# Optimization experiments

Measured on AMD Instinct MI355X. Metric: run time of the kernel, lower is better.

The kernel has to match this reference:

```python
import jax, jax.numpy as jnp
import numpy as np

HIDDEN = 1024
HEADS = 16
HEAD_DIM = HIDDEN // HEADS
SCALE = HEAD_DIM ** -0.5


def setup_inputs() -> dict:
    key = jax.random.key(0)
    ks = jax.random.split(key, 7)
    B, N, T = 4, 64, 128
    x = jax.random.normal(ks[0], (B * N, T, HIDDEN), dtype=jnp.float32)
    bvecs = jax.random.normal(ks[1], (B, T, 3), dtype=jnp.float32)
    w_std = HIDDEN ** -0.5
    qkv_w = jax.random.normal(ks[2], (HIDDEN, 3 * HIDDEN), dtype=jnp.float32) * w_std
    qkv_b = jnp.zeros((3 * HIDDEN,), dtype=jnp.float32)
    proj_w = jax.random.normal(ks[3], (HIDDEN, HIDDEN), dtype=jnp.float32) * w_std
    proj_b = jnp.zeros((HIDDEN,), dtype=jnp.float32)
    angular_bias_scale = jnp.ones((1,), dtype=jnp.float32)
    return {"x": x, "bvecs": bvecs, "qkv_w": qkv_w, "qkv_b": qkv_b,
            "proj_w": proj_w, "proj_b": proj_b,
            "angular_bias_scale": angular_bias_scale}


def reference(x, bvecs, qkv_w, qkv_b, proj_w, proj_b, angular_bias_scale):
    BN, T, D = x.shape
    B = bvecs.shape[0]
    N = BN // B
    # QKV projection -> (3, BN, H, T, hd)
    qkv = (x @ qkv_w + qkv_b).reshape(BN, T, 3, HEADS, HEAD_DIM)
    qkv = jnp.transpose(qkv, (2, 0, 3, 1, 4))
    q, k, v = qkv[0], qkv[1], qkv[2]
    # normalize b-vectors and compute per-batch angular cosine similarity (B, T, T)
    bvecs_n = bvecs / (jnp.linalg.norm(bvecs, axis=-1, keepdims=True) + 1e-6)
    cos_sim = jnp.clip(jnp.einsum('bid,bjd->bij', bvecs_n, bvecs_n), -1.0, 1.0)
    # repeat across the N patches per batch -> (BN, 1, T, T)
    angular_bias = jnp.repeat(cos_sim, N, axis=0)[:, None, :, :]
    attn_logits = jnp.einsum('bhid,bhjd->bhij', q, k) * SCALE
    attn = jax.nn.softmax(attn_logits + angular_bias_scale * angular_bias, axis=-1)
    out = jnp.einsum('bhij,bhjd->bhid', attn, v)
    out = jnp.transpose(out, (0, 2, 1, 3)).reshape(BN, T, D)
    return out @ proj_w + proj_b
```

## Files before the change

### kernel.cpp

```cpp
#include <hip/hip_runtime.h>
#include <hip/hip_bf16.h>
#include <stdint.h>


typedef float f32x4 __attribute__((ext_vector_type(4)));
typedef __bf16 bf16x8 __attribute__((ext_vector_type(8)));
typedef unsigned short us8 __attribute__((ext_vector_type(8)));
typedef unsigned short u16;

#define MROWS 32768

static __device__ __forceinline__ u16 bfbits(float f) {
  __bf16 h = (__bf16)f;
  return __builtin_bit_cast(u16, h);
}
static __device__ __forceinline__ float bff(u16 u) {
  return (float)__builtin_bit_cast(__bf16, u);
}
static __device__ __forceinline__ void gld16(const void* g, void* l) {
  __builtin_amdgcn_global_load_lds(
      (const __attribute__((address_space(1))) void*)g,
      (__attribute__((address_space(3))) void*)l, 16, 0, 0);
}
static __device__ __forceinline__ f32x4 mfma16(bf16x8 a, bf16x8 b, f32x4 c) {
  return __builtin_amdgcn_mfma_f32_16x16x32_bf16(a, b, c, 0, 0, 0);
}

__global__ __launch_bounds__(256) void k_split(const float* __restrict__ x,
                                               u16* __restrict__ xhl, int n4) {
  int i = blockIdx.x * 256 + threadIdx.x;
  if (i >= n4) return;
  float4 v = ((const float4*)x)[i];
  ushort4 h, l;
  h.x = bfbits(v.x); l.x = bfbits(v.x - bff(h.x));
  h.y = bfbits(v.y); l.y = bfbits(v.y - bff(h.y));
  h.z = bfbits(v.z); l.z = bfbits(v.z - bff(h.z));
  h.w = bfbits(v.w); l.w = bfbits(v.w - bff(h.w));
  int i4 = i << 2;
  int r = i4 >> 10, k = i4 & 1023;
  size_t o = ((size_t)r << 11) + (size_t)((k >> 5) << 6) + (k & 31);
  *(ushort4*)(xhl + o) = h;
  *(ushort4*)(xhl + o + 32) = l;
}

__global__ void k_tsplit(const float* __restrict__ w, u16* __restrict__ thl,
                         int K, int N, int remap) {
  __shared__ float tile[32][33];
  int n0 = blockIdx.x * 32, k0 = blockIdx.y * 32;
  int tx = threadIdx.x, ty = threadIdx.y;
#pragma unroll
  for (int j = 0; j < 32; j += 8)
    tile[ty + j][tx] = w[(size_t)(k0 + ty + j) * N + n0 + tx];
  __syncthreads();
#pragma unroll
  for (int j = 0; j < 32; j += 8) {
    float v = tile[tx][ty + j];
    int n = n0 + ty + j;
    int orow = n;
    if (remap) {
      int s = n >> 10, hid = n & 1023;
      orow = (hid >> 8) * 768 + s * 256 + (hid & 255);
    }
    int k = k0 + tx;
    size_t o = ((size_t)orow << 11) + (size_t)((k >> 5) << 6) + (k & 31);
    u16 hb = bfbits(v);
    thl[o] = hb;
    thl[o + 32] = bfbits(v - bff(hb));
  }
}

__global__ void k_gbias(const float* __restrict__ b, float* __restrict__ gb) {
  int n = blockIdx.x * 256 + threadIdx.x;
  if (n >= 3072) return;
  int s = n >> 10, hid = n & 1023;
  gb[(hid >> 8) * 768 + s * 256 + (hid & 255)] = b[n];
}

__global__ void k_cos(const float* __restrict__ bv, float* __restrict__ cosb) {
  int b = blockIdx.x, t = threadIdx.x;
  __shared__ float nb[128][3];
  float x = bv[(b * 128 + t) * 3 + 0];
  float y = bv[(b * 128 + t) * 3 + 1];
  float z = bv[(b * 128 + t) * 3 + 2];
  float inv = 1.0f / (sqrtf(x * x + y * y + z * z) + 1e-6f);
  nb[t][0] = x * inv; nb[t][1] = y * inv; nb[t][2] = z * inv;
  __syncthreads();
  float xn = nb[t][0], yn = nb[t][1], zn = nb[t][2];
  for (int j = 0; j < 128; j++) {
    float c = xn * nb[j][0] + yn * nb[j][1] + zn * nb[j][2];
    c = fminf(1.0f, fmaxf(-1.0f, c));
    cosb[((size_t)b * 128 + t) * 128 + j] = c;
  }
}

template <int AMODE, int MODE>
__global__ __launch_bounds__(512, 2) void k_gemm(
    const u16* __restrict__ Ahl, const float* __restrict__ Af,
    const u16* __restrict__ Bhl, const float* __restrict__ bias,
    float* __restrict__ C) {
  __shared__ __align__(16) u16 sA[3][128 * 64];
  __shared__ __align__(16) u16 sB[3][256 * 64];
  int tid = threadIdx.x;
  int wave = tid >> 6, lane = tid & 63;
  int fr = lane & 15, fq = lane >> 4;
  int wm = wave >> 2, wn = wave & 3;

  int nT = gridDim.y;
  int h = blockIdx.y * gridDim.x + blockIdx.x;
  int nwg = gridDim.x * gridDim.y;
  int w = (h & 7) * (nwg >> 3) + (h >> 3);
  int rowBase = (w / nT) * 128, colBase = (w % nT) * 256;

  f32x4 acc[4][4];
#pragma unroll
  for (int i = 0; i < 4; i++)
#pragma unroll
    for (int j = 0; j < 4; j++) acc[i][j] = (f32x4){0.f, 0.f, 0.f, 0.f};

  int lr = lane >> 3, ls = (lane & 7) ^ lr;
  const u16* aS = Ahl + (size_t)(rowBase + lr) * 2048 + ls * 8;
  const u16* bS = Bhl + (size_t)(colBase + lr) * 2048 + ls * 8;

  auto stageB = [&](int t, int buf) {
#pragma unroll
    for (int q = 0; q < 4; q++) {
      int R = (q * 8 + wave) * 8;
      gld16(bS + (size_t)R * 2048 + t * 64, &sB[buf][R * 64]);
    }
  };
  auto stageA0 = [&](int t, int buf) {
#pragma unroll
    for (int q = 0; q < 2; q++) {
      int R = (q * 8 + wave) * 8;
      gld16(aS + (size_t)R * 2048 + t * 64, &sA[buf][R * 64]);
    }
  };
  auto stageA1 = [&](int t, int buf) {
    int row = tid >> 2, cs = tid & 3;
    const float* src = Af + (size_t)(rowBase + row) * 1024 + t * 32 + cs * 8;
    float4 v0 = *(const float4*)src;
    float4 v1 = *(const float4*)(src + 4);
    float vv[8] = {v0.x, v0.y, v0.z, v0.w, v1.x, v1.y, v1.z, v1.w};
    us8 hv, lv;
#pragma unroll
    for (int i = 0; i < 8; i++) {
      u16 hb = bfbits(vv[i]);
      hv[i] = hb;
      lv[i] = bfbits(vv[i] - bff(hb));
    }
    int sw = row & 7;
    *(us8*)(&sA[buf][row * 64 + ((cs ^ sw) << 3)]) = hv;
    *(us8*)(&sA[buf][row * 64 + (((cs + 4) ^ sw) << 3)]) = lv;
  };
  auto stage = [&](int t, int buf) {
    stageB(t, buf);
    if constexpr (AMODE == 0) stageA0(t, buf);
    else stageA1(t, buf);
  };

  auto tile = [&](int t, int cur, int nbuf, int vmode) {
    const u16* lA = &sA[cur][0];
    const u16* lB = &sB[cur][0];
    bf16x8 fbh[4], fbl[4];
#pragma unroll
    for (int ni = 0; ni < 4; ni++) {
      int c = wn * 64 + ni * 16 + fr;
      int sw = c & 7;
      fbh[ni] = *(const bf16x8*)(&lB[c * 64 + ((fq ^ sw) << 3)]);
      fbl[ni] = *(const bf16x8*)(&lB[c * 64 + (((fq + 4) ^ sw) << 3)]);
    }
    if (t + 2 < 32) stage(t + 2, nbuf);
#pragma unroll
    for (int mi = 0; mi < 4; mi++) {
      bf16x8 fah, fal;
      int r = wm * 64 + mi * 16 + fr;
      int sw = r & 7;
      fah = *(const bf16x8*)(&lA[r * 64 + ((fq ^ sw) << 3)]);
      fal = *(const bf16x8*)(&lA[r * 64 + (((fq + 4) ^ sw) << 3)]);
#pragma unroll
      for (int ni = 0; ni < 4; ni++) {
        acc[mi][ni] = mfma16(fah, fbh[ni], acc[mi][ni]);
        acc[mi][ni] = mfma16(fah, fbl[ni], acc[mi][ni]);
        acc[mi][ni] = mfma16(fal, fbh[ni], acc[mi][ni]);
      }
    }
    if constexpr (AMODE == 1) {
      if (vmode >= 0)
        asm volatile("s_waitcnt vmcnt(0) lgkmcnt(0)" ::: "memory");
    } else {
      if (vmode == 6)
        asm volatile("s_waitcnt vmcnt(6)" ::: "memory");
      else if (vmode == 0)
        asm volatile("s_waitcnt vmcnt(0)" ::: "memory");
    }
    __builtin_amdgcn_s_barrier();
  };

  stage(0, 0);
  stage(1, 1);
  if constexpr (AMODE == 0) {
    asm volatile("s_waitcnt vmcnt(6)" ::: "memory");
  } else {
    asm volatile("s_waitcnt vmcnt(0) lgkmcnt(0)" ::: "memory");
  }
  __builtin_amdgcn_s_barrier();

#pragma unroll 1
  for (int tb = 0; tb < 30; tb += 3) {
    tile(tb, 0, 2, 6);
    tile(tb + 1, 1, 0, 6);
    tile(tb + 2, 2, 1, 6);
  }
  tile(30, 0, 2, 0);
  tile(31, 1, 0, -1);

#pragma unroll
  for (int mi = 0; mi < 4; mi++)
#pragma unroll
    for (int ni = 0; ni < 4; ni++)
#pragma unroll
      for (int rr = 0; rr < 4; rr++) {
        int row = rowBase + wm * 64 + mi * 16 + fq * 4 + rr;
        int col = colBase + wn * 64 + ni * 16 + fr;
        float v = acc[mi][ni][rr] + bias[col];
        if constexpr (MODE == 0) {
          int s = col >> 8, hl2 = (col >> 6) & 3, d = col & 63;
          int bn = row >> 7, t = row & 127;
          size_t idx;
          if (s == 2)
            idx = ((size_t)(bn * 4 + hl2) * 64 + d) * 128 + t;
          else
            idx = ((size_t)(bn * 4 + hl2) * 128 + t) * 64 + d;
          C[(size_t)s * 8388608 + idx] = v;
        } else {
          C[(size_t)row * 1024 + col] = v;
        }
      }
}

__global__ __launch_bounds__(256) void k_attn(
    const float* __restrict__ Q, const float* __restrict__ Kb,
    const float* __restrict__ Vt, const float* __restrict__ cosb,
    const float* __restrict__ absSp, u16* __restrict__ Ohl, int g) {
  __shared__ __align__(16) u16 sQ[2][64 * 72];
  __shared__ __align__(16) u16 sKV[2][64 * 72];
  __shared__ __align__(16) float sS[64 * 132];
  u16* sP = (u16*)sS;

  int bx = blockIdx.x;
  int half = bx & 1, hl = (bx >> 1) & 3, bn = bx >> 3, b = bn >> 6;
  int tid = threadIdx.x, wave = tid >> 6, lane = tid & 63;
  int fr = lane & 15, fq = lane >> 4;
  size_t base = (size_t)(bn * 4 + hl) * 8192;
  float absS = absSp[0];

  {
    const float* src = Q + base + (size_t)half * 4096;
#pragma unroll
    for (int p = 0; p < 4; p++) {
      int f = p * 256 + tid, r = f >> 4, c = f & 15;
      float4 v = *(const float4*)(src + r * 64 + c * 4);
      ushort4 h, l;
      h.x = bfbits(v.x); l.x = bfbits(v.x - bff(h.x));
      h.y = bfbits(v.y); l.y = bfbits(v.y - bff(h.y));
      h.z = bfbits(v.z); l.z = bfbits(v.z - bff(h.z));
      h.w = bfbits(v.w); l.w = bfbits(v.w - bff(h.w));
      *(ushort4*)(&sQ[0][r * 72 + c * 4]) = h;
      *(ushort4*)(&sQ[1][r * 72 + c * 4]) = l;
    }
  }

  bf16x8 qh[2], ql[2];

#pragma unroll
  for (int kt = 0; kt < 2; kt++) {
    if (kt) __syncthreads();
    {
      const float* src = Kb + base + (size_t)kt * 4096;
#pragma unroll
      for (int p = 0; p < 4; p++) {
        int f = p * 256 + tid, r = f >> 4, c = f & 15;
        float4 v = *(const float4*)(src + r * 64 + c * 4);
        ushort4 h, l;
        h.x = bfbits(v.x); l.x = bfbits(v.x - bff(h.x));
        h.y = bfbits(v.y); l.y = bfbits(v.y - bff(h.y));
        h.z = bfbits(v.z); l.z = bfbits(v.z - bff(h.z));
        h.w = bfbits(v.w); l.w = bfbits(v.w - bff(h.w));
        *(ushort4*)(&sKV[0][r * 72 + c * 4]) = h;
        *(ushort4*)(&sKV[1][r * 72 + c * 4]) = l;
      }
    }
    __syncthreads();
    if (kt == 0) {
      int rowl = wave * 16 + fr;
#pragma unroll
      for (int ki = 0; ki < 2; ki++) {
        qh[ki] = *(const bf16x8*)(&sQ[0][rowl * 72 + ki * 32 + fq * 8]);
        ql[ki] = *(const bf16x8*)(&sQ[1][rowl * 72 + ki * 32 + fq * 8]);
      }
    }
#pragma unroll
    for (int nt = 0; nt < 4; nt++) {
      f32x4 a = (f32x4){0.f, 0.f, 0.f, 0.f};
      int cl = nt * 16 + fr;
#pragma unroll
      for (int ki = 0; ki < 2; ki++) {
        bf16x8 kh = *(const bf16x8*)(&sKV[0][cl * 72 + ki * 32 + fq * 8]);
        bf16x8 kl = *(const bf16x8*)(&sKV[1][cl * 72 + ki * 32 + fq * 8]);
        a = mfma16(qh[ki], kh, a);
        a = mfma16(qh[ki], kl, a);
        a = mfma16(ql[ki], kh, a);
      }
#pragma unroll
      for (int rr = 0; rr < 4; rr++) {
        int rl = wave * 16 + fq * 4 + rr;
        int col = kt * 64 + nt * 16 + fr;
        int tg = half * 64 + rl;
        float cv = cosb[((size_t)(b * 128 + tg)) * 128 + col];
        sS[rl * 132 + col] = a[rr] * 0.125f + absS * cv;
      }
    }
  }
  __syncthreads();

  {
    const float* src = Vt + base;
#pragma unroll
    for (int p = 0; p < 4; p++) {
      int f = p * 256 + tid, r = f >> 4, c = f & 15;
      float4 v = *(const float4*)(src + r * 128 + c * 4);
      ushort4 h, l;
      h.x = bfbits(v.x); l.x = bfbits(v.x - bff(h.x));
      h.y = bfbits(v.y); l.y = bfbits(v.y - bff(h.y));
      h.z = bfbits(v.z); l.z = bfbits(v.z - bff(h.z));
      h.w = bfbits(v.w); l.w = bfbits(v.w - bff(h.w));
      *(ushort4*)(&sKV[0][r * 72 + c * 4]) = h;
      *(ushort4*)(&sKV[1][r * 72 + c * 4]) = l;
    }
  }

  for (int r = 0; r < 16; r++) {
    int tl = wave * 16 + r;
    float s0 = sS[tl * 132 + lane], s1 = sS[tl * 132 + 64 + lane];
    float m = fmaxf(s0, s1);
#pragma unroll
    for (int off = 32; off >= 1; off >>= 1) m = fmaxf(m, __shfl_xor(m, off));
    float p0 = __expf(s0 - m), p1 = __expf(s1 - m);
    float sum = p0 + p1;
#pragma unroll
    for (int off = 32; off >= 1; off >>= 1) sum += __shfl_xor(sum, off);
    float inv = 1.0f / sum;
    p0 *= inv; p1 *= inv;
    u16 h0 = bfbits(p0), h1 = bfbits(p1);
    sP[tl * 264 + lane] = h0;
    sP[tl * 264 + 64 + lane] = h1;
    sP[tl * 264 + 128 + lane] = bfbits(p0 - bff(h0));
    sP[tl * 264 + 192 + lane] = bfbits(p1 - bff(h1));
  }

  f32x4 accO[4];
#pragma unroll
  for (int nt = 0; nt < 4; nt++) accO[nt] = (f32x4){0.f, 0.f, 0.f, 0.f};
#pragma unroll
  for (int vt = 0; vt < 2; vt++) {
    if (vt) {
      __syncthreads();
      const float* src = Vt + base + 64;
#pragma unroll
      for (int p = 0; p < 4; p++) {
        int f = p * 256 + tid, r = f >> 4, c = f & 15;
        float4 v = *(const float4*)(src + r * 128 + c * 4);
        ushort4 h, l;
        h.x = bfbits(v.x); l.x = bfbits(v.x - bff(h.x));
        h.y = bfbits(v.y); l.y = bfbits(v.y - bff(h.y));
        h.z = bfbits(v.z); l.z = bfbits(v.z - bff(h.z));
        h.w = bfbits(v.w); l.w = bfbits(v.w - bff(h.w));
        *(ushort4*)(&sKV[0][r * 72 + c * 4]) = h;
        *(ushort4*)(&sKV[1][r * 72 + c * 4]) = l;
      }
    }
    __syncthreads();
    int rowl = wave * 16 + fr;
    bf16x8 ph[2], pl[2];
#pragma unroll
    for (int ki = 0; ki < 2; ki++) {
      ph[ki] = *(const bf16x8*)(&sP[rowl * 264 + vt * 64 + ki * 32 + fq * 8]);
      pl[ki] = *(const bf16x8*)(&sP[rowl * 264 + 128 + vt * 64 + ki * 32 + fq * 8]);
    }
#pragma unroll
    for (int nt = 0; nt < 4; nt++) {
      int d = nt * 16 + fr;
#pragma unroll
      for (int ki = 0; ki < 2; ki++) {
        bf16x8 vh = *(const bf16x8*)(&sKV[0][d * 72 + ki * 32 + fq * 8]);
        bf16x8 vl = *(const bf16x8*)(&sKV[1][d * 72 + ki * 32 + fq * 8]);
        accO[nt] = mfma16(ph[ki], vh, accO[nt]);
        accO[nt] = mfma16(ph[ki], vl, accO[nt]);
        accO[nt] = mfma16(pl[ki], vh, accO[nt]);
      }
    }
  }

  int hg = g * 4 + hl;
#pragma unroll
  for (int nt = 0; nt < 4; nt++)
#pragma unroll
    for (int rr = 0; rr < 4; rr++) {
      int tl = wave * 16 + fq * 4 + rr;
      int tg = half * 64 + tl;
      int d = nt * 16 + fr;
      float v = accO[nt][rr];
      size_t o = ((size_t)(bn * 128 + tg) << 11) +
                 (size_t)(hg * 2 + (d >> 5)) * 64 + (d & 31);
      u16 hh = bfbits(v);
      Ohl[o] = hh;
      Ohl[o + 32] = bfbits(v - bff(hh));
    }
}

extern "C" void kernel_launch(void* const* d_in, const int* in_sizes, int n_in,
                              void* d_out, int out_size, void* d_ws,
                              size_t ws_size, hipStream_t stream) {
  const float* x = (const float*)d_in[0];
  const float* bv = (const float*)d_in[1];
  const float* qkvw = (const float*)d_in[2];
  const float* qkvb = (const float*)d_in[3];
  const float* projw = (const float*)d_in[4];
  const float* projb = (const float*)d_in[5];
  const float* absS = (const float*)d_in[6];
  float* out = (float*)d_out;

  char* ws = (char*)d_ws;
  size_t off = 0;
  auto alloc = [&](size_t b) {
    char* p = ws + off;
    off += (b + 255) & ~(size_t)255;
    return p;
  };
  u16* wqhl = (u16*)alloc((size_t)3072 * 2048 * 2);
  u16* wphl = (u16*)alloc((size_t)1024 * 2048 * 2);
  float* gbias = (float*)alloc(3072 * 4);
  float* cosb = (float*)alloc((size_t)4 * 128 * 128 * 4);
  u16* Ohl = (u16*)alloc((size_t)MROWS * 2048 * 2);
  u16* xhl = (u16*)alloc((size_t)MROWS * 2048 * 2);
  bool planA = (off <= ws_size);

  float* qg = (float*)d_out;

  k_tsplit<<<dim3(96, 32), dim3(32, 8), 0, stream>>>(qkvw, wqhl, 1024, 3072, 1);
  k_tsplit<<<dim3(32, 32), dim3(32, 8), 0, stream>>>(projw, wphl, 1024, 1024, 0);
  k_gbias<<<dim3(12), dim3(256), 0, stream>>>(qkvb, gbias);
  k_cos<<<dim3(4), dim3(128), 0, stream>>>(bv, cosb);
  if (planA)
    k_split<<<dim3(32768), dim3(256), 0, stream>>>(x, xhl, 8388608);

  for (int g = 0; g < 4; g++) {
    const u16* bw = wqhl + (size_t)g * 768 * 2048;
    if (planA)
      k_gemm<0, 0><<<dim3(256, 3), dim3(512), 0, stream>>>(
          xhl, nullptr, bw, gbias + g * 768, qg);
    else
      k_gemm<1, 0><<<dim3(256, 3), dim3(512), 0, stream>>>(
          nullptr, x, bw, gbias + g * 768, qg);
    k_attn<<<dim3(2048), dim3(256), 0, stream>>>(
        qg, qg + 8388608, qg + 16777216, cosb, absS, Ohl, g);
  }

  k_gemm<0, 1><<<dim3(256, 4), dim3(512), 0, stream>>>(
      Ohl, nullptr, wphl, projb, out);
}
```

Measured before the change: 1.275 ms.

## Emit pre-split bf16 hi/lo QKV in swizzled layout and async-load into attention

The QKV GEMM epilogue now writes the bf16 hi/lo split directly into an XOR-swizzled, tile-contiguous layout instead of fp32 arrays. The attention kernel then loads K and V straight into LDS with global_load_lds into double buffers, overlapping the next tile's load with compute. It reads Q fragments directly from global memory. This removes the per-block fp32-to-bf16 splitting and the scalar LDS stores, at the cost of scattered 2-byte stores in the GEMM epilogue.

```diff
diff --git a/kernel.cpp b/kernel.cpp
--- a/kernel.cpp
+++ b/kernel.cpp
@@ -214,6 +214,7 @@
   tile(30, 0, 2, 0);
   tile(31, 1, 0, -1);
 
+  u16* C16 = (u16*)C;
 #pragma unroll
   for (int mi = 0; mi < 4; mi++)
 #pragma unroll
@@ -226,12 +227,19 @@
         if constexpr (MODE == 0) {
           int s = col >> 8, hl2 = (col >> 6) & 3, d = col & 63;
           int bn = row >> 7, t = row & 127;
-          size_t idx;
-          if (s == 2)
-            idx = ((size_t)(bn * 4 + hl2) * 64 + d) * 128 + t;
-          else
-            idx = ((size_t)(bn * 4 + hl2) * 128 + t) * 64 + d;
-          C[(size_t)s * 8388608 + idx] = v;
+          size_t tb_ = (size_t)(bn * 4 + hl2) * 16384;
+          u16 hb = bfbits(v);
+          u16 lb = bfbits(v - bff(hb));
+          size_t o;
+          if (s == 2) {
+            o = (size_t)33554432 + tb_ + (size_t)((t >> 6) << 12) + d * 64 +
+                ((((t >> 3) & 7) ^ (d & 7)) << 3) + (t & 7);
+          } else {
+            o = (size_t)s * 16777216 + tb_ + t * 64 +
+                (((d >> 3) ^ (t & 7)) << 3) + (d & 7);
+          }
+          C16[o] = hb;
+          C16[o + 8192] = lb;
         } else {
           C[(size_t)row * 1024 + col] = v;
         }
@@ -239,11 +247,10 @@
 }
 
 __global__ __launch_bounds__(256) void k_attn(
-    const float* __restrict__ Q, const float* __restrict__ Kb,
-    const float* __restrict__ Vt, const float* __restrict__ cosb,
+    const u16* __restrict__ Qp, const u16* __restrict__ Kp,
+    const u16* __restrict__ Vp, const float* __restrict__ cosb,
     const float* __restrict__ absSp, u16* __restrict__ Ohl, int g) {
-  __shared__ __align__(16) u16 sQ[2][64 * 72];
-  __shared__ __align__(16) u16 sKV[2][64 * 72];
+  __shared__ __align__(16) u16 sKV[2][2][4096];
   __shared__ __align__(16) float sS[64 * 132];
   u16* sP = (u16*)sS;
 
@@ -251,62 +258,60 @@
   int half = bx & 1, hl = (bx >> 1) & 3, bn = bx >> 3, b = bn >> 6;
   int tid = threadIdx.x, wave = tid >> 6, lane = tid & 63;
   int fr = lane & 15, fq = lane >> 4;
-  size_t base = (size_t)(bn * 4 + hl) * 8192;
+  size_t tbase = (size_t)(bn * 4 + hl) * 16384;
   float absS = absSp[0];
 
-  {
-    const float* src = Q + base + (size_t)half * 4096;
-#pragma unroll
-    for (int p = 0; p < 4; p++) {
-      int f = p * 256 + tid, r = f >> 4, c = f & 15;
-      float4 v = *(const float4*)(src + r * 64 + c * 4);
-      ushort4 h, l;
-      h.x = bfbits(v.x); l.x = bfbits(v.x - bff(h.x));
-      h.y = bfbits(v.y); l.y = bfbits(v.y - bff(h.y));
-      h.z = bfbits(v.z); l.z = bfbits(v.z - bff(h.z));
-      h.w = bfbits(v.w); l.w = bfbits(v.w - bff(h.w));
-      *(ushort4*)(&sQ[0][r * 72 + c * 4]) = h;
-      *(ushort4*)(&sQ[1][r * 72 + c * 4]) = l;
-    }
-  }
-
+  const u16* Qt = Qp + tbase;
+  const u16* Kt = Kp + tbase;
+  const u16* Vt = Vp + tbase;
+
+  auto stageK = [&](int kt, int buf) {
+#pragma unroll
+    for (int p2 = 0; p2 < 2; p2++)
+#pragma unroll
+      for (int q = 0; q < 2; q++) {
+        int seg = (q * 4 + wave) * 512;
+        gld16(Kt + p2 * 8192 + kt * 4096 + seg + lane * 8, &sKV[buf][p2][seg]);
+      }
+  };
+  auto stageV = [&](int vt, int buf) {
+#pragma unroll
+    for (int p2 = 0; p2 < 2; p2++)
+#pragma unroll
+      for (int q = 0; q < 2; q++) {
+        int seg = (q * 4 + wave) * 512;
+        gld16(Vt + p2 * 8192 + vt * 4096 + seg + lane * 8, &sKV[buf][p2][seg]);
+      }
+  };
+
+  stageK(0, 0);
+  __builtin_amdgcn_sched_barrier(0);
+  int rowl = wave * 16 + fr;
+  int tq = half * 64 + rowl;
   bf16x8 qh[2], ql[2];
+#pragma unroll
+  for (int ki = 0; ki < 2; ki++) {
+    int sl = ((ki * 4 + fq) ^ (tq & 7)) << 3;
+    qh[ki] = *(const bf16x8*)(Qt + tq * 64 + sl);
+    ql[ki] = *(const bf16x8*)(Qt + 8192 + tq * 64 + sl);
+  }
+  __builtin_amdgcn_sched_barrier(0);
+  stageK(1, 1);
+  __builtin_amdgcn_sched_barrier(0);
+  asm volatile("s_waitcnt vmcnt(4)" ::: "memory");
+  __builtin_amdgcn_s_barrier();
 
 #pragma unroll
   for (int kt = 0; kt < 2; kt++) {
-    if (kt) __syncthreads();
-    {
-      const float* src = Kb + base + (size_t)kt * 4096;
-#pragma unroll
-      for (int p = 0; p < 4; p++) {
-        int f = p * 256 + tid, r = f >> 4, c = f & 15;
-        float4 v = *(const float4*)(src + r * 64 + c * 4);
-        ushort4 h, l;
-        h.x = bfbits(v.x); l.x = bfbits(v.x - bff(h.x));
-        h.y = bfbits(v.y); l.y = bfbits(v.y - bff(h.y));
-        h.z = bfbits(v.z); l.z = bfbits(v.z - bff(h.z));
-        h.w = bfbits(v.w); l.w = bfbits(v.w - bff(h.w));
-        *(ushort4*)(&sKV[0][r * 72 + c * 4]) = h;
-        *(ushort4*)(&sKV[1][r * 72 + c * 4]) = l;
-      }
-    }
-    __syncthreads();
-    if (kt == 0) {
-      int rowl = wave * 16 + fr;
-#pragma unroll
-      for (int ki = 0; ki < 2; ki++) {
-        qh[ki] = *(const bf16x8*)(&sQ[0][rowl * 72 + ki * 32 + fq * 8]);
-        ql[ki] = *(const bf16x8*)(&sQ[1][rowl * 72 + ki * 32 + fq * 8]);
-      }
-    }
 #pragma unroll
     for (int nt = 0; nt < 4; nt++) {
       f32x4 a = (f32x4){0.f, 0.f, 0.f, 0.f};
       int cl = nt * 16 + fr;
 #pragma unroll
       for (int ki = 0; ki < 2; ki++) {
-        bf16x8 kh = *(const bf16x8*)(&sKV[0][cl * 72 + ki * 32 + fq * 8]);
-        bf16x8 kl = *(const bf16x8*)(&sKV[1][cl * 72 + ki * 32 + fq * 8]);
+        int sl = ((ki * 4 + fq) ^ (cl & 7)) << 3;
+        bf16x8 kh = *(const bf16x8*)(&sKV[kt][0][cl * 64 + sl]);
+        bf16x8 kl = *(const bf16x8*)(&sKV[kt][1][cl * 64 + sl]);
         a = mfma16(qh[ki], kh, a);
         a = mfma16(qh[ki], kl, a);
         a = mfma16(ql[ki], kh, a);
@@ -320,24 +325,16 @@
         sS[rl * 132 + col] = a[rr] * 0.125f + absS * cv;
       }
     }
-  }
-  __syncthreads();
-
-  {
-    const float* src = Vt + base;
-#pragma unroll
-    for (int p = 0; p < 4; p++) {
-      int f = p * 256 + tid, r = f >> 4, c = f & 15;
-      float4 v = *(const float4*)(src + r * 128 + c * 4);
-      ushort4 h, l;
-      h.x = bfbits(v.x); l.x = bfbits(v.x - bff(h.x));
-      h.y = bfbits(v.y); l.y = bfbits(v.y - bff(h.y));
-      h.z = bfbits(v.z); l.z = bfbits(v.z - bff(h.z));
-      h.w = bfbits(v.w); l.w = bfbits(v.w - bff(h.w));
-      *(ushort4*)(&sKV[0][r * 72 + c * 4]) = h;
-      *(ushort4*)(&sKV[1][r * 72 + c * 4]) = l;
-    }
-  }
+    __builtin_amdgcn_s_barrier();
+    if (kt == 0) {
+      stageV(0, 0);
+      __builtin_amdgcn_sched_barrier(0);
+      asm volatile("s_waitcnt vmcnt(4)" ::: "memory");
+      __builtin_amdgcn_s_barrier();
+    }
+  }
+  stageV(1, 1);
+  __builtin_amdgcn_sched_barrier(0);
 
   for (int r = 0; r < 16; r++) {
     int tl = wave * 16 + r;
@@ -363,24 +360,12 @@
   for (int nt = 0; nt < 4; nt++) accO[nt] = (f32x4){0.f, 0.f, 0.f, 0.f};
 #pragma unroll
   for (int vt = 0; vt < 2; vt++) {
-    if (vt) {
-      __syncthreads();
-      const float* src = Vt + base + 64;
-#pragma unroll
-      for (int p = 0; p < 4; p++) {
-        int f = p * 256 + tid, r = f >> 4, c = f & 15;
-        float4 v = *(const float4*)(src + r * 128 + c * 4);
-        ushort4 h, l;
-        h.x = bfbits(v.x); l.x = bfbits(v.x - bff(h.x));
-        h.y = bfbits(v.y); l.y = bfbits(v.y - bff(h.y));
-        h.z = bfbits(v.z); l.z = bfbits(v.z - bff(h.z));
-        h.w = bfbits(v.w); l.w = bfbits(v.w - bff(h.w));
-        *(ushort4*)(&sKV[0][r * 72 + c * 4]) = h;
-        *(ushort4*)(&sKV[1][r * 72 + c * 4]) = l;
-      }
-    }
-    __syncthreads();
-    int rowl = wave * 16 + fr;
+    if (vt == 0) {
+      asm volatile("s_waitcnt vmcnt(4)" ::: "memory");
+    } else {
+      asm volatile("s_waitcnt vmcnt(0)" ::: "memory");
+    }
+    __builtin_amdgcn_s_barrier();
     bf16x8 ph[2], pl[2];
 #pragma unroll
     for (int ki = 0; ki < 2; ki++) {
@@ -392,8 +377,9 @@
       int d = nt * 16 + fr;
 #pragma unroll
       for (int ki = 0; ki < 2; ki++) {
-        bf16x8 vh = *(const bf16x8*)(&sKV[0][d * 72 + ki * 32 + fq * 8]);
-        bf16x8 vl = *(const bf16x8*)(&sKV[1][d * 72 + ki * 32 + fq * 8]);
+        int sl = ((ki * 4 + fq) ^ (d & 7)) << 3;
+        bf16x8 vh = *(const bf16x8*)(&sKV[vt][0][d * 64 + sl]);
+        bf16x8 vl = *(const bf16x8*)(&sKV[vt][1][d * 64 + sl]);
         accO[nt] = mfma16(ph[ki], vh, accO[nt]);
         accO[nt] = mfma16(ph[ki], vl, accO[nt]);
         accO[nt] = mfma16(pl[ki], vh, accO[nt]);
@@ -445,7 +431,7 @@
   u16* xhl = (u16*)alloc((size_t)MROWS * 2048 * 2);
   bool planA = (off <= ws_size);
 
-  float* qg = (float*)d_out;
+  u16* O16 = (u16*)d_out;
 
   k_tsplit<<<dim3(96, 32), dim3(32, 8), 0, stream>>>(qkvw, wqhl, 1024, 3072, 1);
   k_tsplit<<<dim3(32, 32), dim3(32, 8), 0, stream>>>(projw, wphl, 1024, 1024, 0);
@@ -458,12 +444,12 @@
     const u16* bw = wqhl + (size_t)g * 768 * 2048;
     if (planA)
       k_gemm<0, 0><<<dim3(256, 3), dim3(512), 0, stream>>>(
-          xhl, nullptr, bw, gbias + g * 768, qg);
+          xhl, nullptr, bw, gbias + g * 768, (float*)O16);
     else
       k_gemm<1, 0><<<dim3(256, 3), dim3(512), 0, stream>>>(
-          nullptr, x, bw, gbias + g * 768, qg);
+          nullptr, x, bw, gbias + g * 768, (float*)O16);
     k_attn<<<dim3(2048), dim3(256), 0, stream>>>(
-        qg, qg + 8388608, qg + 16777216, cosb, absS, Ohl, g);
+        O16, O16 + 16777216, O16 + 33554432, cosb, absS, Ohl, g);
   }
 
   k_gemm<0, 1><<<dim3(256, 4), dim3(512), 0, stream>>>(
```

New measurement: 1.299 ms. Within noise of the previous version (+1.9%).
